# Kernel tuning notes

Measured on AMD Instinct MI355X. Metric: run time of the kernel, lower is better.

The kernel has to match this reference:

```python
import jax, jax.numpy as jnp
import numpy as np

B, LAT, H, K = 8, 128, 1024, 294
N, E = 100000, 1600000
XSIZE = 128.0
TAU = 0.5
STEPS = 3


def setup_inputs() -> dict:
    key = jax.random.key(0)
    ks = jax.random.split(key, 20)
    s_in = 1.0 / np.sqrt(LAT)
    s_h = 1.0 / np.sqrt(H)
    inp = {
        "latent": jax.random.normal(ks[0], (B, LAT), jnp.float32),
        "W0": jax.random.normal(ks[1], (LAT, H), jnp.float32) * s_in,
        "b0": jnp.zeros((H,), jnp.float32),
        "W1": jax.random.normal(ks[2], (H, H), jnp.float32) * s_h,
        "b1": jnp.zeros((H,), jnp.float32),
        "W2": jax.random.normal(ks[3], (H, H), jnp.float32) * s_h,
        "b2": jnp.zeros((H,), jnp.float32),
        "W3": jax.random.normal(ks[4], (H, H), jnp.float32) * s_h,
        "b3": jnp.zeros((H,), jnp.float32),
        # coefficient heads use normal(1e-4) init in the source
        "Wx": jax.random.normal(ks[5], (H, K), jnp.float32) * 1e-4,
        "bx": jnp.zeros((K,), jnp.float32),
        "Wy": jax.random.normal(ks[6], (H, K), jnp.float32) * 1e-4,
        "by": jnp.zeros((K,), jnp.float32),
        "Wz": jax.random.normal(ks[7], (H, K), jnp.float32) * 1e-4,
        "bz": jnp.zeros((K,), jnp.float32),
        # precomputed Zernike/spherical basis evaluated at the N coords: [K, N]
        "Z": jax.random.normal(ks[8], (K, N), jnp.float32),
        "edge_weights": jax.random.uniform(ks[9], (E,), jnp.float32),
        "edge_index": jax.random.randint(ks[10], (2, E), 0, N, jnp.int64),
    }
    return inp


def _decode_coefficients(latent, W0, b0, W1, b1, W2, b2, W3, b3,
                         Wx, bx, Wy, by, Wz, bz):
    h = jax.nn.relu(latent @ W0 + b0)
    for W, b in ((W1, b1), (W2, b2), (W3, b3)):
        h = jax.nn.relu(h + h @ W + b)  # residual MLP block
    return h @ Wx + bx, h @ Wy + by, h @ Wz + bz  # [B, K] each


def _diffuse(flow, edge_index, edge_weights):
    """Graph diffusion smoothing of per-node vectors. flow: [B, N, 3]."""
    src, dst = edge_index[0], edge_index[1]
    deg = jax.ops.segment_sum(edge_weights, dst, num_segments=N)
    deg = jnp.maximum(deg, 1e-6)[:, None, None]  # [N,1,1]
    f = jnp.transpose(flow, (1, 0, 2))  # [N, B, 3]
    w = edge_weights[:, None, None]
    for _ in range(STEPS):
        msg = f[src] * w                                        # gather  [E,B,3]
        agg = jax.ops.segment_sum(msg, dst, num_segments=N)     # scatter [N,B,3]
        f = (1.0 - TAU) * f + TAU * agg / deg
    return jnp.transpose(f, (1, 0, 2))  # [B, N, 3]


def reference(latent, W0, b0, W1, b1, W2, b2, W3, b3,
              Wx, bx, Wy, by, Wz, bz, Z, edge_weights, edge_index):
    cx, cy, cz = _decode_coefficients(latent, W0, b0, W1, b1, W2, b2, W3, b3,
                                      Wx, bx, Wy, by, Wz, bz)
    # basis evaluation: per-axis coefficients contracted with Zernike basis
    dx = jnp.einsum("bk,kn->bn", cx, Z)
    dy = jnp.einsum("bk,kn->bn", cy, Z)
    dz = jnp.einsum("bk,kn->bn", cz, Z)
    flow = (0.5 * XSIZE) * jnp.stack([dx, dy, dz], axis=-1)  # [B, N, 3]
    flow = _diffuse(flow, edge_index, edge_weights)
    reg = 1e-4 * jnp.sqrt(jnp.sum(cx ** 2 + cy ** 2 + cz ** 2))
    return flow, reg
```

## Files before the change

### kernel.cpp

```cpp
#include <hip/hip_runtime.h>
#include <math.h>

#define BB 8
#define LAT 128
#define HH 1024
#define KK 294
#define NN 100000
#define EE 1600000
#define NSTEPS 3
#define XS_HALF 64.0f

#define NB 391
#define CS 8
#define COB 28
#define COB2 30
#define EPT 8
#define EST 200000
#define EBLK 782
#define GON 40

#define F2NB 782
#define KPAD 320
#define GS 80


__device__ __forceinline__ void mlp_part_body(int bid, const float* __restrict__ hin,
                                              const float* __restrict__ W,
                                              float* __restrict__ part, int jdim) {
    int it = bid & 15;
    int bs = bid >> 4;
    int tx = threadIdx.x;
    int il = tx & 63;
    int jg = tx >> 6;
    int i = it * 64 + il;
    int j0 = bs * 64;

    __shared__ float hs[8 * 64];
    for (int u = tx; u < 512; u += 256) {
        int b = u >> 6, lj = u & 63;
        hs[u] = hin[b * jdim + j0 + lj];
    }
    __syncthreads();

    float acc[8];
#pragma unroll
    for (int b = 0; b < 8; ++b) acc[b] = 0.0f;
#pragma unroll
    for (int jj = 0; jj < 16; ++jj) {
        int lj = jg * 16 + jj;
        float w = W[(size_t)(j0 + lj) * HH + i];
#pragma unroll
        for (int b = 0; b < 8; ++b) acc[b] += hs[b * 64 + lj] * w;
    }

    __shared__ float red[4][8][64];
#pragma unroll
    for (int b = 0; b < 8; ++b) red[jg][b][il] = acc[b];
    __syncthreads();
    for (int u = tx; u < 512; u += 256) {
        int b = u >> 6, ii = u & 63;
        float s = red[0][b][ii] + red[1][b][ii] + red[2][b][ii] + red[3][b][ii];
        part[(size_t)bs * 8192 + b * HH + it * 64 + ii] = s;
    }
}

__device__ __forceinline__ void mlp_comb_body(int bid, const float* __restrict__ part,
                                              int nsplit, const float* __restrict__ resid,
                                              const float* __restrict__ bias,
                                              float* __restrict__ hout) {
    int idx = bid * 256 + threadIdx.x;
    if (idx >= BB * HH) return;
    int i = idx & (HH - 1);
    float s = bias[i];
    if (resid) s += resid[idx];
    for (int bs = 0; bs < nsplit; ++bs) s += part[(size_t)bs * 8192 + idx];
    hout[idx] = fmaxf(s, 0.0f);
}

__device__ __forceinline__ void count_body(int bid, const int* __restrict__ ei,
                                           int* __restrict__ cnt, int* __restrict__ rank) {
    int gid = bid * 256 + threadIdx.x;
    if (gid >= EST) return;
    int d[EPT];
#pragma unroll
    for (int j = 0; j < EPT; ++j) d[j] = ei[EE + gid + j * EST];
#pragma unroll
    for (int j = 0; j < EPT; ++j) {
        int p = atomicAdd(&cnt[d[j]], 1);
        rank[gid + j * EST] = p;
    }
}

__device__ __forceinline__ void bsum_body(int bid, const int* __restrict__ cnt,
                                          int* __restrict__ bsum) {
    __shared__ int red[256];
    int i = bid * 256 + threadIdx.x;
    red[threadIdx.x] = (i < NN) ? cnt[i] : 0;
    __syncthreads();
    for (int off = 128; off > 0; off >>= 1) {
        if ((int)threadIdx.x < off) red[threadIdx.x] += red[threadIdx.x + off];
        __syncthreads();
    }
    if (threadIdx.x == 0) bsum[bid] = red[0];
}

__device__ __forceinline__ void bscan_body(const int* __restrict__ bsum,
                                           int* __restrict__ bpre,
                                           int* __restrict__ offs) {
    __shared__ int A[512], Bf[512];
    int t = threadIdx.x;
    A[t] = (t < NB) ? bsum[t] : 0;
    A[t + 256] = (t + 256 < NB) ? bsum[t + 256] : 0;
    __syncthreads();
    int* s = A;
    int* d = Bf;
    for (int off = 1; off < 512; off <<= 1) {
        d[t] = s[t] + ((t >= off) ? s[t - off] : 0);
        int u = t + 256;
        d[u] = s[u] + ((u >= off) ? s[u - off] : 0);
        __syncthreads();
        int* tmp = s; s = d; d = tmp;
    }
    if (t < NB) bpre[t] = (t == 0) ? 0 : s[t - 1];
    int u = t + 256;
    if (u < NB) bpre[u] = s[u - 1];
    if (t == 0) offs[NN] = s[NB - 1];
}

__device__ __forceinline__ void offs_body(int bid, const int* __restrict__ cnt,
                                          const int* __restrict__ bpre,
                                          int* __restrict__ offs) {
    __shared__ int part[256];
    int t = threadIdx.x;
    int i = bid * 256 + t;
    int v = (i < NN) ? cnt[i] : 0;
    part[t] = v;
    __syncthreads();
    for (int off = 1; off < 256; off <<= 1) {
        int u = (t >= off) ? part[t - off] : 0;
        __syncthreads();
        part[t] += u;
        __syncthreads();
    }
    if (i < NN) offs[i] = bpre[bid] + part[t] - v;
}

__device__ __forceinline__ void fill_body(int bid, const int* __restrict__ ei,
                                          const float* __restrict__ ew,
                                          const int* __restrict__ offs,
                                          const int* __restrict__ rank,
                                          int2* __restrict__ csr) {
    int gid = bid * 256 + threadIdx.x;
    if (gid >= EST) return;
    int s[EPT], d[EPT], r[EPT];
    float w[EPT];
#pragma unroll
    for (int j = 0; j < EPT; ++j) {
        int e = gid + j * EST;
        s[j] = ei[e];
        d[j] = ei[EE + e];
        w[j] = ew[e];
        r[j] = rank[e];
    }
#pragma unroll
    for (int j = 0; j < EPT; ++j) {
        int p = offs[d[j]] + r[j];
        int2 v;
        v.x = s[j];
        v.y = __float_as_int(w[j]);
        csr[p] = v;
    }
}

__device__ __forceinline__ void degcsr_body(int bid, const int* __restrict__ offs,
                                            const int2* __restrict__ csr,
                                            float* __restrict__ invh) {
    int n = bid * 256 + threadIdx.x;
    if (n >= NN) return;
    int beg = offs[n], end = offs[n + 1];
    float s = 0.0f;
    for (int i = beg; i < end; ++i) s += __int_as_float(csr[i].y);
    invh[n] = 0.5f / fmaxf(s, 1e-6f);
}

__device__ __forceinline__ void flow2_body(int bid, const float* __restrict__ coefT,
                                           const float* __restrict__ Z,
                                           float* __restrict__ fout) {
    __shared__ float smem[9600];

    int t = threadIdx.x;
    int lane = t & 63;
    int g = t >> 6;
    int gu = __builtin_amdgcn_readfirstlane(g);
    int kb = gu * GS;

    {
        float4* sv = (float4*)smem;
        const float4* cv = (const float4*)coefT;
        for (int u = t; u < KPAD * 6; u += 256) sv[u] = cv[u];
    }
    __syncthreads();

    int n0 = bid * 128;
    int np = n0 + 2 * lane;
    bool valid = (np + 1) < NN;
    int npl = valid ? np : (NN - 2);
    const float* zbase = Z + npl;

    float2 acc[24];
#pragma unroll
    for (int j = 0; j < 24; ++j) acc[j] = make_float2(0.f, 0.f);

    float2 zb[8];
#pragma unroll
    for (int d = 0; d < 8; ++d)
        zb[d] = *(const float2*)(zbase + (size_t)((kb + d) * NN));

    const float4* scv = (const float4*)smem;
    for (int c = 0; c < GS / 8; ++c) {
        int base = c * 8;
#pragma unroll
        for (int d = 0; d < 8; ++d) {
            int kidx = base + d;
            int knl = kb + kidx + 8;
            if (knl > KK - 1) knl = KK - 1;
            float2 zn = *(const float2*)(zbase + (size_t)(knl * NN));
            float4 cc[6];
#pragma unroll
            for (int q = 0; q < 6; ++q) cc[q] = scv[(kb + kidx) * 6 + q];
            const float* cf = (const float*)cc;
#pragma unroll
            for (int j = 0; j < 24; ++j) {
                acc[j].x = fmaf(cf[j], zb[d].x, acc[j].x);
                acc[j].y = fmaf(cf[j], zb[d].y, acc[j].y);
            }
            zb[d] = zn;
        }
    }

    __syncthreads();
    if (g > 0) {
        float2* d = (float2*)(smem + ((g - 1) * 64 + lane) * 50);
#pragma unroll
        for (int j = 0; j < 24; ++j) d[j] = acc[j];
    }
    __syncthreads();
    if (g == 0 && valid) {
#pragma unroll
        for (int s = 0; s < 3; ++s) {
            const float2* r = (const float2*)(smem + (s * 64 + lane) * 50);
#pragma unroll
            for (int j = 0; j < 24; ++j) {
                float2 v = r[j];
                acc[j].x += v.x;
                acc[j].y += v.y;
            }
        }
        float buf[48];
#pragma unroll
        for (int j = 0; j < 24; ++j) {
            buf[j] = XS_HALF * acc[j].x;
            buf[24 + j] = XS_HALF * acc[j].y;
        }
        float4* fr = (float4*)(fout + (size_t)np * 24);
#pragma unroll
        for (int q = 0; q < 12; ++q) fr[q] = ((const float4*)buf)[q];
    }
}

__device__ __forceinline__ void reg_body(const float* __restrict__ coef,
                                         float* __restrict__ out_reg) {
    __shared__ float red[256];
    float s = 0.0f;
    for (int i = threadIdx.x; i < 3 * BB * KK; i += 256) {
        float v = coef[i];
        s += v * v;
    }
    red[threadIdx.x] = s;
    __syncthreads();
    for (int off = 128; off > 0; off >>= 1) {
        if ((int)threadIdx.x < off) red[threadIdx.x] += red[threadIdx.x + off];
        __syncthreads();
    }
    if (threadIdx.x == 0) out_reg[0] = 1e-4f * sqrtf(red[0]);
}


__global__ void K1_mlp0_count(const float* __restrict__ latent, const float* __restrict__ W0,
                              float* __restrict__ part, const int* __restrict__ ei,
                              int* __restrict__ cnt, int* __restrict__ rank) {
    if (blockIdx.x < 32) mlp_part_body(blockIdx.x, latent, W0, part, LAT);
    else count_body(blockIdx.x - 32, ei, cnt, rank);
}

__global__ void K2_comb0_bsum(const float* __restrict__ part, const float* __restrict__ b0,
                              float* __restrict__ hout, const int* __restrict__ cnt,
                              int* __restrict__ bsum) {
    if (blockIdx.x < 32) mlp_comb_body(blockIdx.x, part, 2, nullptr, b0, hout);
    else bsum_body(blockIdx.x - 32, cnt, bsum);
}

__global__ void K3_bscan_mlp1(const int* __restrict__ bsum, int* __restrict__ bpre,
                              int* __restrict__ offs, const float* __restrict__ hin,
                              const float* __restrict__ W1, float* __restrict__ part) {
    if (blockIdx.x == 0) bscan_body(bsum, bpre, offs);
    else mlp_part_body(blockIdx.x - 1, hin, W1, part, HH);
}

__global__ void K4_comb1_offs(const float* __restrict__ part, const float* __restrict__ resid,
                              const float* __restrict__ b1, float* __restrict__ hout,
                              const int* __restrict__ cnt, const int* __restrict__ bpre,
                              int* __restrict__ offs) {
    if (blockIdx.x < 32) mlp_comb_body(blockIdx.x, part, 16, resid, b1, hout);
    else offs_body(blockIdx.x - 32, cnt, bpre, offs);
}

__global__ void K5_mlp2_fill(const float* __restrict__ hin, const float* __restrict__ W2,
                             float* __restrict__ part, const int* __restrict__ ei,
                             const float* __restrict__ ew, const int* __restrict__ offs,
                             const int* __restrict__ rank, int2* __restrict__ csr) {
    if (blockIdx.x < 256) mlp_part_body(blockIdx.x, hin, W2, part, HH);
    else fill_body(blockIdx.x - 256, ei, ew, offs, rank, csr);
}

__global__ void K6_comb2_deg(const float* __restrict__ part, const float* __restrict__ resid,
                             const float* __restrict__ bias, float* __restrict__ hout,
                             const int* __restrict__ offs, const int2* __restrict__ csr,
                             float* __restrict__ invh) {
    if (blockIdx.x < 32) mlp_comb_body(blockIdx.x, part, 16, resid, bias, hout);
    else degcsr_body(blockIdx.x - 32, offs, csr, invh);
}

__global__ void K_mlp_part3(const float* __restrict__ hin, const float* __restrict__ W,
                            float* __restrict__ part) {
    mlp_part_body(blockIdx.x, hin, W, part, HH);
}

__global__ void K_mlp_comb(const float* __restrict__ part, const float* __restrict__ resid,
                           const float* __restrict__ bias, float* __restrict__ hout) {
    mlp_comb_body(blockIdx.x, part, 16, resid, bias, hout);
}

__global__ void k_coef_part(const float* __restrict__ h,
                            const float* __restrict__ Wx,
                            const float* __restrict__ Wy,
                            const float* __restrict__ Wz,
                            float* __restrict__ cpart) {
    int s = blockIdx.x / COB;
    int blk = blockIdx.x % COB;
    int o = blk * 256 + threadIdx.x;
    if (o >= 3 * BB * KK) return;
    int t = o / (BB * KK);
    int r = o % (BB * KK);
    int b = r / KK, k = r % KK;
    const float* W = (t == 0) ? Wx : ((t == 1) ? Wy : Wz);
    const float* hr = h + b * HH;
    int j0 = s * 128;
    float acc = 0.0f;
#pragma unroll 8
    for (int j = 0; j < 128; ++j) acc += hr[j0 + j] * W[(size_t)(j0 + j) * KK + k];
    cpart[(size_t)s * 7056 + o] = acc;
}

__global__ void k_coef_comb(const float* __restrict__ cpart,
                            const float* __restrict__ bx,
                            const float* __restrict__ by,
                            const float* __restrict__ bz,
                            float* __restrict__ coefT) {
    int o = blockIdx.x * 256 + threadIdx.x;
    if (o >= KPAD * 24) return;
    if (o >= 3 * BB * KK) {
        coefT[o] = 0.0f;
        return;
    }
    int t = o / (BB * KK);
    int r = o % (BB * KK);
    int b = r / KK;
    int k = r % KK;
    float s = ((t == 0) ? bx : ((t == 1) ? by : bz))[k];
#pragma unroll
    for (int i = 0; i < CS; ++i) s += cpart[(size_t)i * 7056 + o];
    coefT[k * 24 + b * 3 + t] = s;
}

__global__ void __launch_bounds__(256, 4)
K11_flow_reg(const float* __restrict__ coefT, const float* __restrict__ Z,
             float* __restrict__ fout, float* __restrict__ out_reg) {
    if (blockIdx.x < F2NB) flow2_body(blockIdx.x, coefT, Z, fout);
    else reg_body(coefT, out_reg);
}

__global__ void k_gather(const int* __restrict__ offs, const int2* __restrict__ csr,
                         const float* __restrict__ invh,
                         const float* __restrict__ fin, float* __restrict__ fout) {
    int idx = blockIdx.x * 256 + threadIdx.x;
    if (idx >= NN * 6) return;
    int n = idx / 6;
    int q = idx - n * 6;
    int beg = offs[n], end = offs[n + 1];
    const float4* f4 = (const float4*)fin;
    float4 acc = make_float4(0.f, 0.f, 0.f, 0.f);
    for (int i = beg; i < end; ++i) {
        int2 e = csr[i];
        float w = __int_as_float(e.y);
        float4 fv = f4[(size_t)e.x * 6 + q];
        acc.x += w * fv.x;
        acc.y += w * fv.y;
        acc.z += w * fv.z;
        acc.w += w * fv.w;
    }
    float inv = invh[n];
    float4 fo = f4[(size_t)n * 6 + q];
    float4 r;
    r.x = 0.5f * fo.x + inv * acc.x;
    r.y = 0.5f * fo.y + inv * acc.y;
    r.z = 0.5f * fo.z + inv * acc.z;
    r.w = 0.5f * fo.w + inv * acc.w;
    ((float4*)fout)[(size_t)n * 6 + q] = r;
}

__global__ void k_gather_out(const int* __restrict__ offs, const int2* __restrict__ csr,
                             const float* __restrict__ invh,
                             const float* __restrict__ fin, float* __restrict__ out) {
    __shared__ float ls[GON * 24];
    int t = threadIdx.x;
    int n0 = blockIdx.x * GON;
    if (t < GON * 6) {
        int ln = t / 6, q = t - 6 * ln;
        int n = n0 + ln;
        if (n < NN) {
            int beg = offs[n], end = offs[n + 1];
            const float4* f4 = (const float4*)fin;
            float4 acc = make_float4(0.f, 0.f, 0.f, 0.f);
            for (int i = beg; i < end; ++i) {
                int2 e = csr[i];
                float w = __int_as_float(e.y);
                float4 fv = f4[(size_t)e.x * 6 + q];
                acc.x += w * fv.x;
                acc.y += w * fv.y;
                acc.z += w * fv.z;
                acc.w += w * fv.w;
            }
            float inv = invh[n];
            float4 fo = f4[(size_t)n * 6 + q];
            float* d = &ls[ln * 24 + q * 4];
            d[0] = 0.5f * fo.x + inv * acc.x;
            d[1] = 0.5f * fo.y + inv * acc.y;
            d[2] = 0.5f * fo.z + inv * acc.z;
            d[3] = 0.5f * fo.w + inv * acc.w;
        }
    }
    __syncthreads();
    int cnt = NN - n0; if (cnt > GON) cnt = GON;
    int per_b = cnt * 3;
    for (int b = 0; b < BB; ++b) {
        for (int u = t; u < per_b; u += 256) {
            int n = u / 3;
            int c = u - 3 * n;
            out[(size_t)b * (NN * 3) + (size_t)n0 * 3 + u] = ls[n * 24 + b * 3 + c];
        }
    }
}

extern "C" void kernel_launch(void* const* d_in, const int* in_sizes, int n_in,
                              void* d_out, int out_size, void* d_ws, size_t ws_size,
                              hipStream_t stream) {
    const float* latent = (const float*)d_in[0];
    const float* W0 = (const float*)d_in[1];
    const float* b0 = (const float*)d_in[2];
    const float* W1 = (const float*)d_in[3];
    const float* b1 = (const float*)d_in[4];
    const float* W2 = (const float*)d_in[5];
    const float* b2 = (const float*)d_in[6];
    const float* W3 = (const float*)d_in[7];
    const float* b3 = (const float*)d_in[8];
    const float* Wx = (const float*)d_in[9];
    const float* bx = (const float*)d_in[10];
    const float* Wy = (const float*)d_in[11];
    const float* by = (const float*)d_in[12];
    const float* Wz = (const float*)d_in[13];
    const float* bz = (const float*)d_in[14];
    const float* Z  = (const float*)d_in[15];
    const float* ew = (const float*)d_in[16];
    const int*   ei = (const int*)d_in[17];
    float* out = (float*)d_out;

    float* p = (float*)d_ws;
    float* h_a     = p; p += 8192;
    float* h_b     = p; p += 8192;
    float* hp      = p; p += 16 * 8192;
    float* coef    = p; p += KPAD * 24;
    float* cpart   = p; p += CS * 7056;
    float* invh    = p; p += 100000;
    int*   cnt     = (int*)p; p += 100000;
    int*   offs    = (int*)p; p += 100016;
    int*   bsum    = (int*)p; p += 512;
    int*   bpre    = (int*)p; p += 512;
    int*   rank    = (int*)p; p += 1600000;
    int2*  csr     = (int2*)p; p += 2 * 1600000;
    float* fpart   = p; p += (size_t)2 * NN * 24;

    hipMemsetAsync(cnt, 0, NN * sizeof(int), stream);

    K1_mlp0_count<<<32 + EBLK, 256, 0, stream>>>(latent, W0, hp, ei, cnt, rank);
    K2_comb0_bsum<<<32 + NB, 256, 0, stream>>>(hp, b0, h_a, cnt, bsum);
    K3_bscan_mlp1<<<1 + 256, 256, 0, stream>>>(bsum, bpre, offs, h_a, W1, hp);
    K4_comb1_offs<<<32 + NB, 256, 0, stream>>>(hp, h_a, b1, h_b, cnt, bpre, offs);
    K5_mlp2_fill<<<256 + EBLK, 256, 0, stream>>>(h_b, W2, hp, ei, ew, offs, rank, csr);
    K6_comb2_deg<<<32 + NB, 256, 0, stream>>>(hp, h_b, b2, h_a, offs, csr, invh);
    K_mlp_part3<<<256, 256, 0, stream>>>(h_a, W3, hp);
    K_mlp_comb<<<32, 256, 0, stream>>>(hp, h_a, b3, h_b);
    k_coef_part<<<COB * CS, 256, 0, stream>>>(h_b, Wx, Wy, Wz, cpart);
    k_coef_comb<<<COB2, 256, 0, stream>>>(cpart, bx, by, bz, coef);
    K11_flow_reg<<<F2NB + 1, 256, 0, stream>>>(coef, Z, fpart, out + (size_t)BB * NN * 3);

    float* f0 = fpart;
    float* f1 = fpart + (size_t)NN * 24;
    k_gather<<<(NN * 6 + 255) / 256, 256, 0, stream>>>(offs, csr, invh, f0, f1);
    k_gather<<<(NN * 6 + 255) / 256, 256, 0, stream>>>(offs, csr, invh, f1, f0);
    k_gather_out<<<(NN + GON - 1) / GON, 256, 0, stream>>>(offs, csr, invh, f0, out);
}
```

Before: 547.4 us.

## Read flow coefficients from constant memory and prefetch CSR entries in gathers

Coefficients are copied device-to-device into a __constant__ buffer so the flow kernel reads them through scalar constant loads, since the index is wave-uniform. This drops the shared-memory staging and its block barrier. Separately, the gather kernels now software-prefetch the next CSR entry to overlap index loads with feature loads. It adds one extra memcpy in the stream, and constant-cache behaviour for this access pattern is uncertain.

New measurement: 540.3 us. About the same (-1.3%).

```diff
diff --git a/kernel.cpp b/kernel.cpp
--- a/kernel.cpp
+++ b/kernel.cpp
@@ -22,6 +22,8 @@
 #define F2NB 782
 #define KPAD 320
 #define GS 80
+
+__constant__ float ccoefT[KPAD * 24];
 
 
 __device__ __forceinline__ void mlp_part_body(int bid, const float* __restrict__ hin,
@@ -183,8 +185,7 @@
     invh[n] = 0.5f / fmaxf(s, 1e-6f);
 }
 
-__device__ __forceinline__ void flow2_body(int bid, const float* __restrict__ coefT,
-                                           const float* __restrict__ Z,
+__device__ __forceinline__ void flow2_body(int bid, const float* __restrict__ Z,
                                            float* __restrict__ fout) {
     __shared__ float smem[9600];
 
@@ -194,13 +195,6 @@
     int gu = __builtin_amdgcn_readfirstlane(g);
     int kb = gu * GS;
 
-    {
-        float4* sv = (float4*)smem;
-        const float4* cv = (const float4*)coefT;
-        for (int u = t; u < KPAD * 6; u += 256) sv[u] = cv[u];
-    }
-    __syncthreads();
-
     int n0 = bid * 128;
     int np = n0 + 2 * lane;
     bool valid = (np + 1) < NN;
@@ -216,19 +210,15 @@
     for (int d = 0; d < 8; ++d)
         zb[d] = *(const float2*)(zbase + (size_t)((kb + d) * NN));
 
-    const float4* scv = (const float4*)smem;
     for (int c = 0; c < GS / 8; ++c) {
-        int base = c * 8;
+        int base = kb + c * 8;
 #pragma unroll
         for (int d = 0; d < 8; ++d) {
-            int kidx = base + d;
-            int knl = kb + kidx + 8;
+            int k = base + d;
+            int knl = k + 8;
             if (knl > KK - 1) knl = KK - 1;
-            float2 zn = *(const float2*)(zbase + (size_t)(knl * NN));
-            float4 cc[6];
-#pragma unroll
-            for (int q = 0; q < 6; ++q) cc[q] = scv[(kb + kidx) * 6 + q];
-            const float* cf = (const float*)cc;
+            float2 zn = *(const float2*)(zbase + (size_t)knl * NN);
+            const float* cf = &ccoefT[k * 24];
 #pragma unroll
             for (int j = 0; j < 24; ++j) {
                 acc[j].x = fmaf(cf[j], zb[d].x, acc[j].x);
@@ -386,7 +376,7 @@
 __global__ void __launch_bounds__(256, 4)
 K11_flow_reg(const float* __restrict__ coefT, const float* __restrict__ Z,
              float* __restrict__ fout, float* __restrict__ out_reg) {
-    if (blockIdx.x < F2NB) flow2_body(blockIdx.x, coefT, Z, fout);
+    if (blockIdx.x < F2NB) flow2_body(blockIdx.x, Z, fout);
     else reg_body(coefT, out_reg);
 }
 
@@ -400,14 +390,18 @@
     int beg = offs[n], end = offs[n + 1];
     const float4* f4 = (const float4*)fin;
     float4 acc = make_float4(0.f, 0.f, 0.f, 0.f);
-    for (int i = beg; i < end; ++i) {
-        int2 e = csr[i];
-        float w = __int_as_float(e.y);
-        float4 fv = f4[(size_t)e.x * 6 + q];
-        acc.x += w * fv.x;
-        acc.y += w * fv.y;
-        acc.z += w * fv.z;
-        acc.w += w * fv.w;
+    if (beg < end) {
+        int2 e = csr[beg];
+        for (int i = beg; i < end; ++i) {
+            int2 en = (i + 1 < end) ? csr[i + 1] : e;
+            float w = __int_as_float(e.y);
+            float4 fv = f4[(size_t)e.x * 6 + q];
+            acc.x += w * fv.x;
+            acc.y += w * fv.y;
+            acc.z += w * fv.z;
+            acc.w += w * fv.w;
+            e = en;
+        }
     }
     float inv = invh[n];
     float4 fo = f4[(size_t)n * 6 + q];
@@ -432,14 +426,18 @@
             int beg = offs[n], end = offs[n + 1];
             const float4* f4 = (const float4*)fin;
             float4 acc = make_float4(0.f, 0.f, 0.f, 0.f);
-            for (int i = beg; i < end; ++i) {
-                int2 e = csr[i];
-                float w = __int_as_float(e.y);
-                float4 fv = f4[(size_t)e.x * 6 + q];
-                acc.x += w * fv.x;
-                acc.y += w * fv.y;
-                acc.z += w * fv.z;
-                acc.w += w * fv.w;
+            if (beg < end) {
+                int2 e = csr[beg];
+                for (int i = beg; i < end; ++i) {
+                    int2 en = (i + 1 < end) ? csr[i + 1] : e;
+                    float w = __int_as_float(e.y);
+                    float4 fv = f4[(size_t)e.x * 6 + q];
+                    acc.x += w * fv.x;
+                    acc.y += w * fv.y;
+                    acc.z += w * fv.z;
+                    acc.w += w * fv.w;
+                    e = en;
+                }
             }
             float inv = invh[n];
             float4 fo = f4[(size_t)n * 6 + q];
@@ -512,6 +510,8 @@
     K_mlp_comb<<<32, 256, 0, stream>>>(hp, h_a, b3, h_b);
     k_coef_part<<<COB * CS, 256, 0, stream>>>(h_b, Wx, Wy, Wz, cpart);
     k_coef_comb<<<COB2, 256, 0, stream>>>(cpart, bx, by, bz, coef);
+    hipMemcpyToSymbolAsync(HIP_SYMBOL(ccoefT), coef, KPAD * 24 * sizeof(float), 0,
+                           hipMemcpyDeviceToDevice, stream);
     K11_flow_reg<<<F2NB + 1, 256, 0, stream>>>(coef, Z, fpart, out + (size_t)BB * NN * 3);
 
     float* f0 = fpart;
```
